# Kernel tuning notes

Hardware: AMD Instinct MI355X
Metric: run time of the kernel (lower is better)

Reference implementation:

```python
import jax, jax.numpy as jnp
import numpy as np


def _conv3x3(x, w, b):
    # x: [B,C,H,W], w: [O,C,3,3], b: [O]; stride 1, padding 1 (SAME)
    y = jax.lax.conv_general_dilated(
        x, w, window_strides=(1, 1), padding='SAME',
        dimension_numbers=('NCHW', 'OIHW', 'NCHW'))
    return y + b[None, :, None, None]


def setup_inputs() -> dict:
    key = jax.random.key(0)
    ks = jax.random.split(key, 7)
    B, C, H, W = 8, 256, 48, 48
    emb = 512
    fan_out = emb * 9  # kaiming_normal_ fan_out, relu gain sqrt(2)
    std = float(np.sqrt(2.0 / fan_out))
    feat = jax.random.normal(ks[0], (B, C, H, W), dtype=jnp.float32)
    Wq = jax.random.normal(ks[1], (emb, C, 3, 3), dtype=jnp.float32) * std
    Wk = jax.random.normal(ks[2], (emb, C, 3, 3), dtype=jnp.float32) * std
    Wv = jax.random.normal(ks[3], (emb, C, 3, 3), dtype=jnp.float32) * std
    bound = 1.0 / np.sqrt(C * 9)
    bq = jax.random.uniform(ks[4], (emb,), jnp.float32, -bound, bound)
    bk = jax.random.uniform(ks[5], (emb,), jnp.float32, -bound, bound)
    bv = jax.random.uniform(ks[6], (emb,), jnp.float32, -bound, bound)
    return {"feat": feat, "Wq": Wq, "bq": bq, "Wk": Wk, "bk": bk, "Wv": Wv, "bv": bv}


def reference(feat, Wq, bq, Wk, bk, Wv, bv):
    B, C, H, W = feat.shape
    emb = Wq.shape[0]
    q = _conv3x3(feat, Wq, bq).reshape(B, emb, H * W)  # [B,E,N]
    k = _conv3x3(feat, Wk, bk).reshape(B, emb, H * W)
    v = _conv3x3(feat, Wv, bv).reshape(B, emb, H * W)
    # att[b,i,j] = <q[:, i], k[:, j]>, softmax over j (keys)
    att = jnp.einsum('bei,bej->bij', q, k)
    att = jax.nn.softmax(att, axis=2)
    # v_att[b,e,i] = sum_j v[b,e,j] * att[b,i,j]
    v_att = jnp.einsum('bej,bij->bei', v, att)
    return v_att.reshape(B, emb, H, W) + v.reshape(B, emb, H, W)
```

## Files before the change

kernel.cpp:

```cpp
#include <hip/hip_runtime.h>


typedef _Float16 f16;
typedef _Float16 f16x4 __attribute__((ext_vector_type(4)));
typedef _Float16 f16x8 __attribute__((ext_vector_type(8)));
typedef float    f32x4  __attribute__((ext_vector_type(4)));
typedef float    f32x16 __attribute__((ext_vector_type(16)));

__device__ __forceinline__ f32x16 mfma16(f16x8 a, f16x8 b, f32x16 c) {
  return __builtin_amdgcn_mfma_f32_32x32x16_f16(a, b, c, 0, 0, 0);
}

#define NB   8
#define NC   256
#define NH   48
#define NN   2304
#define NE   512
#define HP   50
#define QSTR 528


__global__ void pack_feat(const float* __restrict__ x, f16* __restrict__ p) {
  int idx = blockIdx.x * 256 + threadIdx.x;
  int c  = idx & 255;
  int q  = idx >> 8;
  int xp = q % 50; int t = q / 50; int yp = t % 50; int b = t / 50;
  float v = 0.f;
  if (yp >= 1 && yp <= 48 && xp >= 1 && xp <= 48)
    v = x[((b * NC + c) * NH + (yp - 1)) * NH + (xp - 1)];
  p[idx] = (f16)v;
}

__global__ void pack_w(const float* __restrict__ wq, const float* __restrict__ wk,
                       const float* __restrict__ wv,
                       f16* __restrict__ oq, f16* __restrict__ ok,
                       f16* __restrict__ ov) {
  int idx = blockIdx.x * 256 + threadIdx.x;
  int c = idx & 255;
  int r = idx >> 8;
  int e = r & 511; int t = r >> 9;
  int src = (e * NC + c) * 9 + t;
  int cc = c >> 4, cl = c & 15, et = e >> 5, el = e & 31;
  int dst = ((cc * 9 + t) * 16 + et) * 512 + el * 16 + cl;
  oq[dst] = (f16)wq[src];
  ok[dst] = (f16)wk[src];
  ov[dst] = (f16)wv[src];
}

__global__ __launch_bounds__(256, 2) void conv3_qkv(
    const f16* __restrict__ xh,
    const f16* __restrict__ wq, const f16* __restrict__ wk,
    const f16* __restrict__ wv,
    const float* __restrict__ bq, const float* __restrict__ bk,
    const float* __restrict__ bv,
    f16* __restrict__ oq, f16* __restrict__ kf, f16* __restrict__ vf) {
  __shared__ __align__(16) f16 sx[12000];

  const int tid = threadIdx.x;
  const int lane = tid & 63, wvx = tid >> 6;
  const int l31 = lane & 31;
  const int koff = (lane >> 5) * 8;
  const int et = blockIdx.x;
  const int e0 = et * 32;
  const int by = blockIdx.y;
  const int b = by / 6, strip = by % 6;
  const int y0 = strip * 8;

  int pb[3];
#pragma unroll
  for (int nt = 0; nt < 3; ++nt) {
    int n = wvx * 96 + nt * 32 + l31;
    pb[nt] = (n / 48) * 50 + (n % 48);
  }

  int sgp[4], sgo[4]; bool sok[4]; int gbase[4];
#pragma unroll
  for (int u = 0; u < 4; ++u) {
    int g = u * 256 + tid;
    sok[u] = (g < 1000);
    int gg = sok[u] ? g : 999;
    sgp[u] = gg >> 1; sgo[u] = (gg & 1) * 8;
    int row = sgp[u] / 50, xx = sgp[u] % 50;
    gbase[u] = ((b * HP + y0 + row) * HP + xx) * NC + sgo[u];
  }

  f32x16 acc[3][3];
#pragma unroll
  for (int f = 0; f < 3; ++f)
#pragma unroll
    for (int nt = 0; nt < 3; ++nt)
#pragma unroll
      for (int i = 0; i < 16; ++i) acc[f][nt][i] = 0.f;

  f16x8 rx[4];
#pragma unroll
  for (int u = 0; u < 4; ++u)
    rx[u] = *(const f16x8*)(xh + gbase[u]);

  const int wlocal = l31 * 16 + koff;

  for (int cc = 0; cc < 16; ++cc) {
    __syncthreads();
#pragma unroll
    for (int u = 0; u < 4; ++u)
      if (sok[u]) *(f16x8*)(sx + sgp[u] * 24 + sgo[u]) = rx[u];
    __syncthreads();
    if (cc < 15) {
      int c0 = (cc + 1) * 16;
#pragma unroll
      for (int u = 0; u < 4; ++u)
        rx[u] = *(const f16x8*)(xh + gbase[u] + c0);
    }
#pragma unroll
    for (int t = 0; t < 9; ++t) {
      const int dy = t / 3, dx = t % 3;
      const int dpo = (dy * 50 + dx) * 24 + koff;
      f16x8 bh[3];
#pragma unroll
      for (int nt = 0; nt < 3; ++nt)
        bh[nt] = *(const f16x8*)(sx + pb[nt] * 24 + dpo);
      int wb = ((cc * 9 + t) * 16 + et) * 512 + wlocal;
      f16x8 aq = *(const f16x8*)(wq + wb);
      f16x8 ak = *(const f16x8*)(wk + wb);
      f16x8 av = *(const f16x8*)(wv + wb);
#pragma unroll
      for (int nt = 0; nt < 3; ++nt) {
        acc[0][nt] = mfma16(aq, bh[nt], acc[0][nt]);
        acc[1][nt] = mfma16(ak, bh[nt], acc[1][nt]);
        acc[2][nt] = mfma16(av, bh[nt], acc[2][nt]);
      }
    }
  }

  const int colh = (lane >> 5) * 4;
#pragma unroll
  for (int nt = 0; nt < 3; ++nt) {
    int n = wvx * 96 + nt * 32 + l31;
    int pos = (y0 + n / 48) * 48 + (n % 48);
    const int jblk = pos >> 5, jl = pos & 31;
    const int jc = pos >> 4, lhv = (pos >> 3) & 1, uv = pos & 7;
#pragma unroll
    for (int g = 0; g < 4; ++g) {
      int eb = e0 + g * 8 + colh;
      f32x4 sq = *(const f32x4*)(bq + eb);
      f32x4 sk = *(const f32x4*)(bk + eb);
      f32x4 sv = *(const f32x4*)(bv + eb);
      f16x4 hq, hk;
#pragma unroll
      for (int j = 0; j < 4; ++j) {
        hq[j] = (f16)(acc[0][nt][g * 4 + j] + sq[j]);
        hk[j] = (f16)(acc[1][nt][g * 4 + j] + sk[j]);
        int e = eb + j;
        vf[((((size_t)b * 16 + (e >> 5)) * 144 + jc) * 64 + lhv * 32 + (e & 31)) * 8 + uv] =
            (f16)(acc[2][nt][g * 4 + j] + sv[j]);
      }
      *(f16x4*)(kf + ((((size_t)b * 72 + jblk) * 32 + (eb >> 4)) * 64 +
                      ((eb >> 3) & 1) * 32 + jl) * 8 + (eb & 7)) = hk;
      *(f16x4*)(oq + ((size_t)b * NN + pos) * NE + eb) = hq;
    }
  }
}

__global__ __launch_bounds__(256, 3) void attn(
    const f16* __restrict__ qt, const f16* __restrict__ kf,
    const f16* __restrict__ vf, float* __restrict__ out) {
  __shared__ __align__(16) f16 q_lds[32 * QSTR];
  __shared__ __align__(16) f16 sP2[4096];
  __shared__ __align__(16) float s_pmax[128];
  __shared__ __align__(16) float s_psum[128];

  const int tid = threadIdx.x;
  const int lane = tid & 63, wvx = tid >> 6;
  const int l31 = lane & 31, lh = lane >> 5;
  const int bid = blockIdx.x;
  const int b = bid & 7;
  const int i0 = (bid >> 3) * 32;

  {
    const f16* qb = qt + ((size_t)b * NN + i0) * NE;
#pragma unroll
    for (int it = 0; it < 8; ++it) {
      int g = it * 256 + tid;
      int row = g >> 6, gr = g & 63;
      f16x8 v = *(const f16x8*)(qb + row * NE + gr * 8);
      int sgr = (gr & ~7) | ((gr & 7) ^ (row & 7));
      *(f16x8*)(q_lds + row * QSTR + sgr * 8) = v;
    }
  }
  __syncthreads();

  float m_reg = -1e30f, l_reg = 0.f;
  f32x16 O[4];
#pragma unroll
  for (int nt = 0; nt < 4; ++nt)
#pragma unroll
    for (int i = 0; i < 16; ++i) O[nt][i] = 0.f;

  const int x7 = l31 & 7;
  const f16* kfw = kf + (size_t)(b * 72 + wvx) * 16384 + lane * 8;
  const f16* vfw = vf + (size_t)(b * 16 + wvx * 4) * 73728 + lane * 8;
  const f16* qrow = q_lds + l31 * QSTR;

  for (int jt = 0; jt < 18; ++jt) {
    const f16* kfl = kfw + (size_t)jt * 4 * 16384;
    f32x16 S0, S1;
#pragma unroll
    for (int i = 0; i < 16; ++i) { S0[i] = 0.f; S1[i] = 0.f; }
    f16x8 kpipe[6];
#pragma unroll
    for (int t = 0; t < 6; ++t) kpipe[t] = *(const f16x8*)(kfl + t * 512);
    f16x8 qpipe[2];
#pragma unroll
    for (int t = 0; t < 2; ++t) {
      int ga = t * 2 + lh;
      int sg = (ga & ~7) | ((ga & 7) ^ x7);
      qpipe[t] = *(const f16x8*)(qrow + sg * 8);
    }
#pragma unroll
    for (int c = 0; c < 32; ++c) {
      f16x8 ak = kpipe[c % 6];
      if (c + 6 < 32) kpipe[c % 6] = *(const f16x8*)(kfl + (c + 6) * 512);
      f16x8 aq = qpipe[c & 1];
      if (c + 2 < 32) {
        int ga = (c + 2) * 2 + lh;
        int sg = (ga & ~7) | ((ga & 7) ^ x7);
        qpipe[c & 1] = *(const f16x8*)(qrow + sg * 8);
      }
      if (c & 1) S1 = mfma16(ak, aq, S1);
      else       S0 = mfma16(ak, aq, S0);
    }
    f32x16 S;
#pragma unroll
    for (int r = 0; r < 16; ++r) S[r] = S0[r] + S1[r];

    float wmax = S[0];
#pragma unroll
    for (int r = 1; r < 16; ++r) wmax = fmaxf(wmax, S[r]);
    wmax = fmaxf(wmax, __shfl_xor(wmax, 32, 64));
    if (lane < 32) s_pmax[l31 * 4 + wvx] = wmax;
    __syncthreads();
    f32x4 pm4 = *(const f32x4*)(s_pmax + l31 * 4);
    float gmax = fmaxf(fmaxf(pm4[0], pm4[1]), fmaxf(pm4[2], pm4[3]));
    float mnew = fmaxf(m_reg, gmax);
    float alpha = __expf(m_reg - mnew);
    m_reg = mnew;

    f16 ph[16];
    float psum = 0.f;
#pragma unroll
    for (int r = 0; r < 16; ++r) {
      f16 p = (f16)__expf(S[r] - mnew);
      ph[r] = p;
      psum += (float)p;
    }
    union Q4 { f16x4 h; int i2[2]; };
    Q4 q4[4];
#pragma unroll
    for (int t = 0; t < 4; ++t)
#pragma unroll
      for (int u = 0; u < 4; ++u) q4[t].h[u] = ph[t * 4 + u];
#pragma unroll
    for (int ks = 0; ks < 2; ++ks) {
      Q4 t1, t2;
      t1.i2[0] = __shfl_xor(q4[2 * ks + 1].i2[0], 32, 64);
      t1.i2[1] = __shfl_xor(q4[2 * ks + 1].i2[1], 32, 64);
      t2.i2[0] = __shfl_xor(q4[2 * ks].i2[0], 32, 64);
      t2.i2[1] = __shfl_xor(q4[2 * ks].i2[1], 32, 64);
      f16x4 first  = lh ? t1.h : q4[2 * ks].h;
      f16x4 second = lh ? q4[2 * ks + 1].h : t2.h;
      f16x8 frag;
#pragma unroll
      for (int u = 0; u < 4; ++u) { frag[u] = first[u]; frag[4 + u] = second[u]; }
      *(f16x8*)(sP2 + ((wvx * 2 + ks) * 64 + lane) * 8) = frag;
    }
    psum += __shfl_xor(psum, 32, 64);
    if (lane < 32) s_psum[l31 * 4 + wvx] = psum;
#pragma unroll
    for (int nt = 0; nt < 4; ++nt)
#pragma unroll
      for (int r = 0; r < 16; ++r) O[nt][r] *= alpha;
    __syncthreads();
    f32x4 ps4 = *(const f32x4*)(s_psum + l31 * 4);
    l_reg = l_reg * alpha + (ps4[0] + ps4[1] + ps4[2] + ps4[3]);

    const f16* vfl = vfw + (size_t)jt * 8 * 512;
    f16x8 vpipe[6];
#pragma unroll
    for (int t = 0; t < 6; ++t) {
      int nt = t & 3, cg = t >> 2;
      vpipe[t] = *(const f16x8*)(vfl + (size_t)nt * 73728 + cg * 512);
    }
    f16x8 apc = *(const f16x8*)(sP2 + (0 * 64 + lane) * 8);
    f16x8 apn = *(const f16x8*)(sP2 + (1 * 64 + lane) * 8);
#pragma unroll
    for (int c = 0; c < 32; ++c) {
      int nt = c & 3, cg = c >> 2;
      f16x8 av = vpipe[c % 6];
      if (c + 6 < 32) {
        int nt2 = (c + 6) & 3, cg2 = (c + 6) >> 2;
        vpipe[c % 6] = *(const f16x8*)(vfl + (size_t)nt2 * 73728 + cg2 * 512);
      }
      O[nt] = mfma16(av, apc, O[nt]);
      if (nt == 3) {
        apc = apn;
        if (cg + 2 < 8) apn = *(const f16x8*)(sP2 + ((cg + 2) * 64 + lane) * 8);
      }
    }
  }

  float inv = 1.0f / l_reg;
  const int ii = i0 + l31;
  const int jcR = ii >> 4, lhR = (ii >> 3) & 1, uR = ii & 7;
#pragma unroll
  for (int nt = 0; nt < 4; ++nt) {
    const f16* vres = vf + ((((size_t)(b * 16 + wvx * 4 + nt)) * 144 + jcR) * 64 + lhR * 32) * 8 + uR;
    const int ebase = wvx * 128 + nt * 32;
#pragma unroll
    for (int r = 0; r < 16; ++r) {
      int el = (r & 3) + 8 * (r >> 2) + 4 * lh;
      float rv = (float)vres[el * 8];
      out[((size_t)b * NE + ebase + el) * NN + ii] = O[nt][r] * inv + rv;
    }
  }
}

extern "C" void kernel_launch(void* const* d_in, const int* in_sizes, int n_in,
                              void* d_out, int out_size, void* d_ws, size_t ws_size,
                              hipStream_t stream) {
  const float* feat = (const float*)d_in[0];
  const float* Wq = (const float*)d_in[1];
  const float* bq = (const float*)d_in[2];
  const float* Wk = (const float*)d_in[3];
  const float* bk = (const float*)d_in[4];
  const float* Wv = (const float*)d_in[5];
  const float* bv = (const float*)d_in[6];
  float* out = (float*)d_out;

  char* ws = (char*)d_ws;
  size_t off = 0;
  auto alloc = [&](size_t bytes) {
    void* p = ws + off;
    off += (bytes + 255) & ~(size_t)255;
    return p;
  };
  const size_t FP = (size_t)NB * HP * HP * NC;
  const size_t WP = (size_t)9 * NE * NC;
  const size_t QP = (size_t)NB * NN * NE;
  f16* fp  = (f16*)alloc(FP * 2);
  f16* wq  = (f16*)alloc(WP * 2);
  f16* wk  = (f16*)alloc(WP * 2);
  f16* wv  = (f16*)alloc(WP * 2);
  f16* q_t = (f16*)alloc(QP * 2);
  f16* k_f = (f16*)alloc(QP * 2);
  f16* v_f = (f16*)alloc(QP * 2);

  pack_feat<<<dim3(FP / 256), dim3(256), 0, stream>>>(feat, fp);
  pack_w<<<dim3(WP / 256), dim3(256), 0, stream>>>(Wq, Wk, Wv, wq, wk, wv);

  conv3_qkv<<<dim3(16, 48), dim3(256), 0, stream>>>(
      fp, wq, wk, wv, bq, bk, bv, q_t, k_f, v_f);

  attn<<<dim3(576), dim3(256), 0, stream>>>(q_t, k_f, v_f, out);
}
```

Baseline: 447.5 us.

## Overlap next-tile QK^T MFMAs with current-tile PV in attention loop

Restructures the attention loop so the QK^T MFMAs for key tile jt+1 run interleaved with the PV MFMAs for tile jt. The softmax probability buffer and the max/sum reduction buffers are double-buffered so the two stages do not overwrite each other across barriers. Q in LDS is stored in MFMA fragment order, read without the XOR swizzle, and the O/l rescale is skipped when no row max changes. The goal is to hide softmax latency and memory stalls behind matrix work, at the cost of more registers and LDS that could limit the 3-blocks-per-CU occupancy.

```diff
diff --git a/kernel.cpp b/kernel.cpp
--- a/kernel.cpp
+++ b/kernel.cpp
@@ -17,7 +17,6 @@
 #define NN   2304
 #define NE   512
 #define HP   50
-#define QSTR 528
 
 
 __global__ void pack_feat(const float* __restrict__ x, f16* __restrict__ p) {
@@ -164,10 +163,10 @@
 __global__ __launch_bounds__(256, 3) void attn(
     const f16* __restrict__ qt, const f16* __restrict__ kf,
     const f16* __restrict__ vf, float* __restrict__ out) {
-  __shared__ __align__(16) f16 q_lds[32 * QSTR];
-  __shared__ __align__(16) f16 sP2[4096];
-  __shared__ __align__(16) float s_pmax[128];
-  __shared__ __align__(16) float s_psum[128];
+  __shared__ __align__(16) f16 q_lds[16384];
+  __shared__ __align__(16) f16 sP2[8192];
+  __shared__ __align__(16) float s_pmax[256];
+  __shared__ __align__(16) float s_psum[256];
 
   const int tid = threadIdx.x;
   const int lane = tid & 63, wvx = tid >> 6;
@@ -183,8 +182,7 @@
       int g = it * 256 + tid;
       int row = g >> 6, gr = g & 63;
       f16x8 v = *(const f16x8*)(qb + row * NE + gr * 8);
-      int sgr = (gr & ~7) | ((gr & 7) ^ (row & 7));
-      *(f16x8*)(q_lds + row * QSTR + sgr * 8) = v;
+      *(f16x8*)(q_lds + (gr >> 1) * 512 + (gr & 1) * 256 + row * 8) = v;
     }
   }
   __syncthreads();
@@ -196,55 +194,58 @@
 #pragma unroll
     for (int i = 0; i < 16; ++i) O[nt][i] = 0.f;
 
-  const int x7 = l31 & 7;
   const f16* kfw = kf + (size_t)(b * 72 + wvx) * 16384 + lane * 8;
   const f16* vfw = vf + (size_t)(b * 16 + wvx * 4) * 73728 + lane * 8;
-  const f16* qrow = q_lds + l31 * QSTR;
-
-  for (int jt = 0; jt < 18; ++jt) {
-    const f16* kfl = kfw + (size_t)jt * 4 * 16384;
-    f32x16 S0, S1;
-#pragma unroll
-    for (int i = 0; i < 16; ++i) { S0[i] = 0.f; S1[i] = 0.f; }
-    f16x8 kpipe[6];
-#pragma unroll
-    for (int t = 0; t < 6; ++t) kpipe[t] = *(const f16x8*)(kfl + t * 512);
-    f16x8 qpipe[2];
-#pragma unroll
-    for (int t = 0; t < 2; ++t) {
-      int ga = t * 2 + lh;
-      int sg = (ga & ~7) | ((ga & 7) ^ x7);
-      qpipe[t] = *(const f16x8*)(qrow + sg * 8);
-    }
+  const f16* qlw = q_lds + lane * 8;
+
+  f32x16 S0, S1;
+#pragma unroll
+  for (int i = 0; i < 16; ++i) { S0[i] = 0.f; S1[i] = 0.f; }
+
+  {
+    const f16* kfl = kfw;
+    f16x8 kp[3];
+#pragma unroll
+    for (int t = 0; t < 3; ++t) kp[t] = *(const f16x8*)(kfl + t * 512);
 #pragma unroll
     for (int c = 0; c < 32; ++c) {
-      f16x8 ak = kpipe[c % 6];
-      if (c + 6 < 32) kpipe[c % 6] = *(const f16x8*)(kfl + (c + 6) * 512);
-      f16x8 aq = qpipe[c & 1];
-      if (c + 2 < 32) {
-        int ga = (c + 2) * 2 + lh;
-        int sg = (ga & ~7) | ((ga & 7) ^ x7);
-        qpipe[c & 1] = *(const f16x8*)(qrow + sg * 8);
-      }
+      f16x8 ak = kp[c % 3];
+      if (c + 3 < 32) kp[c % 3] = *(const f16x8*)(kfl + (c + 3) * 512);
+      f16x8 aq = *(const f16x8*)(qlw + c * 512);
       if (c & 1) S1 = mfma16(ak, aq, S1);
       else       S0 = mfma16(ak, aq, S0);
     }
+  }
+
+  for (int jt = 0; jt < 18; ++jt) {
+    const int t = jt;
     f32x16 S;
 #pragma unroll
     for (int r = 0; r < 16; ++r) S[r] = S0[r] + S1[r];
-
     float wmax = S[0];
 #pragma unroll
     for (int r = 1; r < 16; ++r) wmax = fmaxf(wmax, S[r]);
     wmax = fmaxf(wmax, __shfl_xor(wmax, 32, 64));
-    if (lane < 32) s_pmax[l31 * 4 + wvx] = wmax;
+    if (lane < 32) s_pmax[(t & 1) * 128 + l31 * 4 + wvx] = wmax;
     __syncthreads();
-    f32x4 pm4 = *(const f32x4*)(s_pmax + l31 * 4);
+
+    f32x4 pm4 = *(const f32x4*)(s_pmax + (t & 1) * 128 + l31 * 4);
     float gmax = fmaxf(fmaxf(pm4[0], pm4[1]), fmaxf(pm4[2], pm4[3]));
+    if (t > 0) {
+      f32x4 ps4 = *(const f32x4*)(s_psum + ((t - 1) & 1) * 128 + l31 * 4);
+      l_reg += ps4[0] + ps4[1] + ps4[2] + ps4[3];
+    }
     float mnew = fmaxf(m_reg, gmax);
-    float alpha = __expf(m_reg - mnew);
-    m_reg = mnew;
-
+    if (!__all(mnew == m_reg)) {
+      float alpha = __expf(m_reg - mnew);
+      l_reg *= alpha;
+      m_reg = mnew;
+#pragma unroll
+      for (int nt = 0; nt < 4; ++nt)
+#pragma unroll
+        for (int r = 0; r < 16; ++r) O[nt][r] *= alpha;
+    }
+    f16* spw = sP2 + (t & 1) * 4096;
     f16 ph[16];
     float psum = 0.f;
 #pragma unroll
@@ -256,9 +257,9 @@
     union Q4 { f16x4 h; int i2[2]; };
     Q4 q4[4];
 #pragma unroll
-    for (int t = 0; t < 4; ++t)
-#pragma unroll
-      for (int u = 0; u < 4; ++u) q4[t].h[u] = ph[t * 4 + u];
+    for (int t4 = 0; t4 < 4; ++t4)
+#pragma unroll
+      for (int u = 0; u < 4; ++u) q4[t4].h[u] = ph[t4 * 4 + u];
 #pragma unroll
     for (int ks = 0; ks < 2; ++ks) {
       Q4 t1, t2;
@@ -271,43 +272,71 @@
       f16x8 frag;
 #pragma unroll
       for (int u = 0; u < 4; ++u) { frag[u] = first[u]; frag[4 + u] = second[u]; }
-      *(f16x8*)(sP2 + ((wvx * 2 + ks) * 64 + lane) * 8) = frag;
+      *(f16x8*)(spw + ((wvx * 2 + ks) * 64 + lane) * 8) = frag;
     }
     psum += __shfl_xor(psum, 32, 64);
-    if (lane < 32) s_psum[l31 * 4 + wvx] = psum;
-#pragma unroll
-    for (int nt = 0; nt < 4; ++nt)
-#pragma unroll
-      for (int r = 0; r < 16; ++r) O[nt][r] *= alpha;
+    if (lane < 32) s_psum[(t & 1) * 128 + l31 * 4 + wvx] = psum;
     __syncthreads();
-    f32x4 ps4 = *(const f32x4*)(s_psum + l31 * 4);
-    l_reg = l_reg * alpha + (ps4[0] + ps4[1] + ps4[2] + ps4[3]);
-
-    const f16* vfl = vfw + (size_t)jt * 8 * 512;
-    f16x8 vpipe[6];
-#pragma unroll
-    for (int t = 0; t < 6; ++t) {
-      int nt = t & 3, cg = t >> 2;
-      vpipe[t] = *(const f16x8*)(vfl + (size_t)nt * 73728 + cg * 512);
-    }
-    f16x8 apc = *(const f16x8*)(sP2 + (0 * 64 + lane) * 8);
-    f16x8 apn = *(const f16x8*)(sP2 + (1 * 64 + lane) * 8);
-#pragma unroll
-    for (int c = 0; c < 32; ++c) {
-      int nt = c & 3, cg = c >> 2;
-      f16x8 av = vpipe[c % 6];
-      if (c + 6 < 32) {
-        int nt2 = (c + 6) & 3, cg2 = (c + 6) >> 2;
-        vpipe[c % 6] = *(const f16x8*)(vfl + (size_t)nt2 * 73728 + cg2 * 512);
+
+    const f16* vfl = vfw + (size_t)t * 4096;
+    const f16* spc = spw;
+    if (jt < 17) {
+      const f16* kfl = kfw + (size_t)(jt + 1) * 4 * 16384;
+#pragma unroll
+      for (int r = 0; r < 16; ++r) { S0[r] = 0.f; S1[r] = 0.f; }
+      f16x8 kp[3], vp[3];
+#pragma unroll
+      for (int p = 0; p < 3; ++p) kp[p] = *(const f16x8*)(kfl + p * 512);
+#pragma unroll
+      for (int p = 0; p < 3; ++p)
+        vp[p] = *(const f16x8*)(vfl + (size_t)(p & 3) * 73728 + (p >> 2) * 512);
+      f16x8 ap0 = *(const f16x8*)(spc + lane * 8);
+      f16x8 ap1 = *(const f16x8*)(spc + (64 + lane) * 8);
+#pragma unroll
+      for (int c = 0; c < 32; ++c) {
+        f16x8 ak = kp[c % 3];
+        if (c + 3 < 32) kp[c % 3] = *(const f16x8*)(kfl + (c + 3) * 512);
+        f16x8 av = vp[c % 3];
+        if (c + 3 < 32) {
+          int c2 = c + 3;
+          vp[c % 3] = *(const f16x8*)(vfl + (size_t)(c2 & 3) * 73728 + (c2 >> 2) * 512);
+        }
+        f16x8 aq = *(const f16x8*)(qlw + c * 512);
+        if (c & 1) S1 = mfma16(ak, aq, S1);
+        else       S0 = mfma16(ak, aq, S0);
+        O[c & 3] = mfma16(av, ap0, O[c & 3]);
+        if ((c & 3) == 3) {
+          ap0 = ap1;
+          if ((c >> 2) < 6) ap1 = *(const f16x8*)(spc + (((c >> 2) + 2) * 64 + lane) * 8);
+        }
       }
-      O[nt] = mfma16(av, apc, O[nt]);
-      if (nt == 3) {
-        apc = apn;
-        if (cg + 2 < 8) apn = *(const f16x8*)(sP2 + ((cg + 2) * 64 + lane) * 8);
+    } else {
+      f16x8 vp[3];
+#pragma unroll
+      for (int p = 0; p < 3; ++p)
+        vp[p] = *(const f16x8*)(vfl + (size_t)(p & 3) * 73728 + (p >> 2) * 512);
+      f16x8 ap0 = *(const f16x8*)(spc + lane * 8);
+      f16x8 ap1 = *(const f16x8*)(spc + (64 + lane) * 8);
+#pragma unroll
+      for (int c = 0; c < 32; ++c) {
+        f16x8 av = vp[c % 3];
+        if (c + 3 < 32) {
+          int c2 = c + 3;
+          vp[c % 3] = *(const f16x8*)(vfl + (size_t)(c2 & 3) * 73728 + (c2 >> 2) * 512);
+        }
+        O[c & 3] = mfma16(av, ap0, O[c & 3]);
+        if ((c & 3) == 3) {
+          ap0 = ap1;
+          if ((c >> 2) < 6) ap1 = *(const f16x8*)(spc + (((c >> 2) + 2) * 64 + lane) * 8);
+        }
       }
     }
   }
 
+  {
+    f32x4 ps4 = *(const f32x4*)(s_psum + 128 + l31 * 4);
+    l_reg += ps4[0] + ps4[1] + ps4[2] + ps4[3];
+  }
   float inv = 1.0f / l_reg;
   const int ii = i0 + l31;
   const int jcR = ii >> 4, lhR = (ii >> 3) & 1, uR = ii & 7;
```

New measurement: 907.2 us. 103% more time.

## Split fused QKV conv into three per-projection kernels with weight prefetch

Applied to the files above, without the earlier changes.

Replaces the single conv kernel that computed Q, K and V together with a templated kernel launched three times, once per projection. Each launch keeps a third of the accumulators, raises the launch-bounds occupancy target from 2 to 3 blocks per SM, and prefetches the next tap's weights one step ahead. In exchange the input feature tiles are loaded into LDS three times instead of once, and there are two extra kernel launches, each grid of 768 blocks.

```diff
diff --git a/kernel.cpp b/kernel.cpp
--- a/kernel.cpp
+++ b/kernel.cpp
@@ -47,13 +47,10 @@
   ov[dst] = (f16)wv[src];
 }
 
-__global__ __launch_bounds__(256, 2) void conv3_qkv(
-    const f16* __restrict__ xh,
-    const f16* __restrict__ wq, const f16* __restrict__ wk,
-    const f16* __restrict__ wv,
-    const float* __restrict__ bq, const float* __restrict__ bk,
-    const float* __restrict__ bv,
-    f16* __restrict__ oq, f16* __restrict__ kf, f16* __restrict__ vf) {
+template<int F>
+__global__ __launch_bounds__(256, 3) void conv3_one(
+    const f16* __restrict__ xh, const f16* __restrict__ w,
+    const float* __restrict__ bias, f16* __restrict__ o) {
   __shared__ __align__(16) f16 sx[12000];
 
   const int tid = threadIdx.x;
@@ -84,13 +81,11 @@
     gbase[u] = ((b * HP + y0 + row) * HP + xx) * NC + sgo[u];
   }
 
-  f32x16 acc[3][3];
-#pragma unroll
-  for (int f = 0; f < 3; ++f)
-#pragma unroll
-    for (int nt = 0; nt < 3; ++nt)
-#pragma unroll
-      for (int i = 0; i < 16; ++i) acc[f][nt][i] = 0.f;
+  f32x16 acc[3];
+#pragma unroll
+  for (int nt = 0; nt < 3; ++nt)
+#pragma unroll
+    for (int i = 0; i < 16; ++i) acc[nt][i] = 0.f;
 
   f16x8 rx[4];
 #pragma unroll
@@ -111,23 +106,18 @@
       for (int u = 0; u < 4; ++u)
         rx[u] = *(const f16x8*)(xh + gbase[u] + c0);
     }
+    f16x8 wf = *(const f16x8*)(w + ((cc * 9 + 0) * 16 + et) * 512 + wlocal);
 #pragma unroll
     for (int t = 0; t < 9; ++t) {
+      f16x8 wcur = wf;
+      if (t < 8)
+        wf = *(const f16x8*)(w + ((cc * 9 + t + 1) * 16 + et) * 512 + wlocal);
       const int dy = t / 3, dx = t % 3;
       const int dpo = (dy * 50 + dx) * 24 + koff;
-      f16x8 bh[3];
-#pragma unroll
-      for (int nt = 0; nt < 3; ++nt)
-        bh[nt] = *(const f16x8*)(sx + pb[nt] * 24 + dpo);
-      int wb = ((cc * 9 + t) * 16 + et) * 512 + wlocal;
-      f16x8 aq = *(const f16x8*)(wq + wb);
-      f16x8 ak = *(const f16x8*)(wk + wb);
-      f16x8 av = *(const f16x8*)(wv + wb);
 #pragma unroll
       for (int nt = 0; nt < 3; ++nt) {
-        acc[0][nt] = mfma16(aq, bh[nt], acc[0][nt]);
-        acc[1][nt] = mfma16(ak, bh[nt], acc[1][nt]);
-        acc[2][nt] = mfma16(av, bh[nt], acc[2][nt]);
+        f16x8 bh = *(const f16x8*)(sx + pb[nt] * 24 + dpo);
+        acc[nt] = mfma16(wcur, bh, acc[nt]);
       }
     }
   }
@@ -142,21 +132,26 @@
 #pragma unroll
     for (int g = 0; g < 4; ++g) {
       int eb = e0 + g * 8 + colh;
-      f32x4 sq = *(const f32x4*)(bq + eb);
-      f32x4 sk = *(const f32x4*)(bk + eb);
-      f32x4 sv = *(const f32x4*)(bv + eb);
-      f16x4 hq, hk;
-#pragma unroll
-      for (int j = 0; j < 4; ++j) {
-        hq[j] = (f16)(acc[0][nt][g * 4 + j] + sq[j]);
-        hk[j] = (f16)(acc[1][nt][g * 4 + j] + sk[j]);
-        int e = eb + j;
-        vf[((((size_t)b * 16 + (e >> 5)) * 144 + jc) * 64 + lhv * 32 + (e & 31)) * 8 + uv] =
-            (f16)(acc[2][nt][g * 4 + j] + sv[j]);
-      }
-      *(f16x4*)(kf + ((((size_t)b * 72 + jblk) * 32 + (eb >> 4)) * 64 +
-                      ((eb >> 3) & 1) * 32 + jl) * 8 + (eb & 7)) = hk;
-      *(f16x4*)(oq + ((size_t)b * NN + pos) * NE + eb) = hq;
+      f32x4 sb = *(const f32x4*)(bias + eb);
+      if constexpr (F == 0) {
+        f16x4 hq;
+#pragma unroll
+        for (int j = 0; j < 4; ++j) hq[j] = (f16)(acc[nt][g * 4 + j] + sb[j]);
+        *(f16x4*)(o + ((size_t)b * NN + pos) * NE + eb) = hq;
+      } else if constexpr (F == 1) {
+        f16x4 hk;
+#pragma unroll
+        for (int j = 0; j < 4; ++j) hk[j] = (f16)(acc[nt][g * 4 + j] + sb[j]);
+        *(f16x4*)(o + ((((size_t)b * 72 + jblk) * 32 + (eb >> 4)) * 64 +
+                       ((eb >> 3) & 1) * 32 + jl) * 8 + (eb & 7)) = hk;
+      } else {
+#pragma unroll
+        for (int j = 0; j < 4; ++j) {
+          int e = eb + j;
+          o[((((size_t)b * 16 + (e >> 5)) * 144 + jc) * 64 + lhv * 32 + (e & 31)) * 8 + uv] =
+              (f16)(acc[nt][g * 4 + j] + sb[j]);
+        }
+      }
     }
   }
 }
@@ -357,8 +352,9 @@
   pack_feat<<<dim3(FP / 256), dim3(256), 0, stream>>>(feat, fp);
   pack_w<<<dim3(WP / 256), dim3(256), 0, stream>>>(Wq, Wk, Wv, wq, wk, wv);
 
-  conv3_qkv<<<dim3(16, 48), dim3(256), 0, stream>>>(
-      fp, wq, wk, wv, bq, bk, bv, q_t, k_f, v_f);
+  conv3_one<0><<<dim3(16, 48), dim3(256), 0, stream>>>(fp, wq, bq, q_t);
+  conv3_one<1><<<dim3(16, 48), dim3(256), 0, stream>>>(fp, wk, bk, k_f);
+  conv3_one<2><<<dim3(16, 48), dim3(256), 0, stream>>>(fp, wv, bv, v_f);
 
   attn<<<dim3(576), dim3(256), 0, stream>>>(q_t, k_f, v_f, out);
 }
```

Result: no change. 456.0 us (+1.9%).
